# Kernel tuning notes

Measured on AMD Instinct MI355X. Metric: run time of the kernel, lower is better.

The kernel has to match this reference:

```python
import jax, jax.numpy as jnp
import numpy as np

MARGIN = 0.5
EPS = 1e-6  # torch F.pairwise_distance eps, added to the difference


def _make_indices(B, seed=0):
    rng = np.random.default_rng(seed)
    i1 = np.empty(B, dtype=np.int64)
    i2 = np.empty(B, dtype=np.int64)
    for i in range(B):
        a, b = rng.choice(B, size=2, replace=False)
        while a == i or b == i:
            a, b = rng.choice(B, size=2, replace=False)
        i1[i], i2[i] = a, b
    return i1, i2


def setup_inputs() -> dict:
    key = jax.random.key(0)
    k1, k2 = jax.random.split(key)
    B, D = 8192, 4096
    features = jax.random.normal(k1, (B, D), dtype=jnp.float32)
    label = jax.random.uniform(k2, (B, 1), dtype=jnp.float32) * 200.0  # bone-age-like months
    i1, i2 = _make_indices(B)
    return {
        "features": features,
        "label": label,
        "idx1": jnp.asarray(i1),
        "idx2": jnp.asarray(i2),
    }


def reference(features, label, idx1, idx2):
    # features: [B, D], label: [B, 1]
    a = features
    t1 = features[idx1]                                   # [B, D]
    t2 = features[idx2]                                   # [B, D]
    # L1Loss(reduction='sum') on per-sample labels
    d1 = jnp.sum(jnp.abs(label - label[idx1]), axis=-1)   # [B]
    d2 = jnp.sum(jnp.abs(label - label[idx2]), axis=-1)   # [B]
    # if d1 >= d2: near = t2, far = t1 else near = t1, far = t2
    swap = (d1 >= d2)[:, None]
    near = jnp.where(swap, t2, t1)
    far = jnp.where(swap, t1, t2)
    # TripletMarginLoss(margin=0.5, p=2); per-sample inputs are 1-D vectors,
    # so each call's 'mean' reduction is over a single element (identity).
    dn = jnp.sqrt(jnp.sum((a - near + EPS) ** 2, axis=-1))  # [B]
    df = jnp.sqrt(jnp.sum((a - far + EPS) ** 2, axis=-1))   # [B]
    per_sample = jnp.maximum(dn - df + MARGIN, 0.0)
    # loss is always >= 0, so the `if loss >= 0` accumulates every sample.
    return jnp.sum(per_sample)
```

## Files before the change

kernel.cpp:

```cpp
#include <hip/hip_runtime.h>

#define FEAT_D 4096
#define MARGIN_F 0.5f
#define EPS_F 1e-6f

__global__ __launch_bounds__(256) void triplet_loss_kernel(
    const float* __restrict__ features,
    const float* __restrict__ label,
    const int* __restrict__ idx1,
    const int* __restrict__ idx2,
    float* __restrict__ partials)
{
    const int row = blockIdx.x;
    const int tid = threadIdx.x;
    const int i1 = idx1[row];
    const int i2 = idx2[row];

    const float4* a  = reinterpret_cast<const float4*>(features + (size_t)row * FEAT_D) + tid;
    const float4* t1 = reinterpret_cast<const float4*>(features + (size_t)i1  * FEAT_D) + tid;
    const float4* t2 = reinterpret_cast<const float4*>(features + (size_t)i2  * FEAT_D) + tid;

    float s1 = 0.f, s2 = 0.f;
#pragma unroll
    for (int k = 0; k < 4; ++k) {
        const float4 va = a[k * 256];
        const float4 v1 = t1[k * 256];
        const float4 v2 = t2[k * 256];
        float d;
        d = va.x - v1.x + EPS_F; s1 += d * d;
        d = va.y - v1.y + EPS_F; s1 += d * d;
        d = va.z - v1.z + EPS_F; s1 += d * d;
        d = va.w - v1.w + EPS_F; s1 += d * d;
        d = va.x - v2.x + EPS_F; s2 += d * d;
        d = va.y - v2.y + EPS_F; s2 += d * d;
        d = va.z - v2.z + EPS_F; s2 += d * d;
        d = va.w - v2.w + EPS_F; s2 += d * d;
    }

#pragma unroll
    for (int off = 32; off > 0; off >>= 1) {
        s1 += __shfl_down(s1, off, 64);
        s2 += __shfl_down(s2, off, 64);
    }

    __shared__ float sh1[4], sh2[4];
    const int wave = tid >> 6;
    const int lane = tid & 63;
    if (lane == 0) { sh1[wave] = s1; sh2[wave] = s2; }
    __syncthreads();

    if (tid == 0) {
        const float S1 = sh1[0] + sh1[1] + sh1[2] + sh1[3];
        const float S2 = sh2[0] + sh2[1] + sh2[2] + sh2[3];
        const float lab = label[row];
        const float d1 = fabsf(lab - label[i1]);
        const float d2 = fabsf(lab - label[i2]);
        const bool swap = (d1 >= d2);
        const float sn = swap ? S2 : S1;
        const float sf = swap ? S1 : S2;
        const float loss = fmaxf(sqrtf(sn) - sqrtf(sf) + MARGIN_F, 0.f);
        partials[row] = loss;
    }
}

__global__ __launch_bounds__(256) void reduce_kernel(
    const float* __restrict__ partials, float* __restrict__ out, int n)
{
    const int tid = threadIdx.x;
    float s = 0.f;
    const float4* p4 = reinterpret_cast<const float4*>(partials);
    for (int i = tid; i < n / 4; i += 256) {
        const float4 v = p4[i];
        s += (v.x + v.y) + (v.z + v.w);
    }
#pragma unroll
    for (int off = 32; off > 0; off >>= 1)
        s += __shfl_down(s, off, 64);

    __shared__ float sh[4];
    const int wave = tid >> 6;
    const int lane = tid & 63;
    if (lane == 0) sh[wave] = s;
    __syncthreads();
    if (tid == 0) out[0] = sh[0] + sh[1] + sh[2] + sh[3];
}

extern "C" void kernel_launch(void* const* d_in, const int* in_sizes, int n_in,
                              void* d_out, int out_size, void* d_ws, size_t ws_size,
                              hipStream_t stream) {
    const float* features = (const float*)d_in[0];
    const float* label    = (const float*)d_in[1];
    const int*   idx1     = (const int*)d_in[2];
    const int*   idx2     = (const int*)d_in[3];
    float* out      = (float*)d_out;
    float* partials = (float*)d_ws;

    const int B = in_sizes[1];

    triplet_loss_kernel<<<B, 256, 0, stream>>>(features, label, idx1, idx2, partials);
    reduce_kernel<<<1, 256, 0, stream>>>(partials, out, B);
}
```

Before: 67.40 us.

## Process four rows per block with double-buffered register prefetch

Each block now handles four anchor rows and loads the next row's anchor and two target rows into a second register buffer while the current row is reduced. Sched barriers keep the load issue ahead of the compute. The goal is more memory-level parallelism per wave and less per-block launch and sync overhead. The cost is higher register pressure from 24 float4 buffers, and a quarter as many blocks. The final reduction kernel is also widened to 1024 threads.

```diff
diff --git a/kernel.cpp b/kernel.cpp
--- a/kernel.cpp
+++ b/kernel.cpp
@@ -3,6 +3,8 @@
 #define FEAT_D 4096
 #define MARGIN_F 0.5f
 #define EPS_F 1e-6f
+#define ROWS_PER_BLK 4
+
 
 __global__ __launch_bounds__(256) void triplet_loss_kernel(
     const float* __restrict__ features,
@@ -11,65 +13,86 @@
     const int* __restrict__ idx2,
     float* __restrict__ partials)
 {
-    const int row = blockIdx.x;
     const int tid = threadIdx.x;
-    const int i1 = idx1[row];
-    const int i2 = idx2[row];
+    const int row0 = blockIdx.x * ROWS_PER_BLK;
 
-    const float4* a  = reinterpret_cast<const float4*>(features + (size_t)row * FEAT_D) + tid;
-    const float4* t1 = reinterpret_cast<const float4*>(features + (size_t)i1  * FEAT_D) + tid;
-    const float4* t2 = reinterpret_cast<const float4*>(features + (size_t)i2  * FEAT_D) + tid;
+    __shared__ float sh1[ROWS_PER_BLK][4], sh2[ROWS_PER_BLK][4];
 
-    float s1 = 0.f, s2 = 0.f;
-#pragma unroll
-    for (int k = 0; k < 4; ++k) {
-        const float4 va = a[k * 256];
-        const float4 v1 = t1[k * 256];
-        const float4 v2 = t2[k * 256];
-        float d;
-        d = va.x - v1.x + EPS_F; s1 += d * d;
-        d = va.y - v1.y + EPS_F; s1 += d * d;
-        d = va.z - v1.z + EPS_F; s1 += d * d;
-        d = va.w - v1.w + EPS_F; s1 += d * d;
-        d = va.x - v2.x + EPS_F; s2 += d * d;
-        d = va.y - v2.y + EPS_F; s2 += d * d;
-        d = va.z - v2.z + EPS_F; s2 += d * d;
-        d = va.w - v2.w + EPS_F; s2 += d * d;
+    float4 bufA[12], bufB[12];
+
+#define ISSUE(BUF, R)                                                          \
+    {                                                                          \
+        const int rr_ = (R);                                                   \
+        const int j1_ = idx1[rr_], j2_ = idx2[rr_];                            \
+        const float4* pa_ = reinterpret_cast<const float4*>(features + (size_t)rr_ * FEAT_D) + tid; \
+        const float4* p1_ = reinterpret_cast<const float4*>(features + (size_t)j1_ * FEAT_D) + tid; \
+        const float4* p2_ = reinterpret_cast<const float4*>(features + (size_t)j2_ * FEAT_D) + tid; \
+        _Pragma("unroll")                                                      \
+        for (int k = 0; k < 4; ++k) BUF[k]     = pa_[k * 256];                 \
+        _Pragma("unroll")                                                      \
+        for (int k = 0; k < 4; ++k) BUF[4 + k] = p1_[k * 256];                 \
+        _Pragma("unroll")                                                      \
+        for (int k = 0; k < 4; ++k) BUF[8 + k] = p2_[k * 256];                 \
+    }                                                                          \
+    __builtin_amdgcn_sched_barrier(0);
+
+#define COMPUTE(BUF, SLOT)                                                     \
+    {                                                                          \
+        float s1_ = 0.f, s2_ = 0.f;                                            \
+        _Pragma("unroll")                                                      \
+        for (int k = 0; k < 4; ++k) {                                          \
+            float d_;                                                          \
+            d_ = BUF[k].x - BUF[4+k].x + EPS_F; s1_ += d_ * d_;                \
+            d_ = BUF[k].y - BUF[4+k].y + EPS_F; s1_ += d_ * d_;                \
+            d_ = BUF[k].z - BUF[4+k].z + EPS_F; s1_ += d_ * d_;                \
+            d_ = BUF[k].w - BUF[4+k].w + EPS_F; s1_ += d_ * d_;                \
+            d_ = BUF[k].x - BUF[8+k].x + EPS_F; s2_ += d_ * d_;                \
+            d_ = BUF[k].y - BUF[8+k].y + EPS_F; s2_ += d_ * d_;                \
+            d_ = BUF[k].z - BUF[8+k].z + EPS_F; s2_ += d_ * d_;                \
+            d_ = BUF[k].w - BUF[8+k].w + EPS_F; s2_ += d_ * d_;                \
+        }                                                                      \
+        _Pragma("unroll")                                                      \
+        for (int off = 32; off > 0; off >>= 1) {                               \
+            s1_ += __shfl_down(s1_, off, 64);                                  \
+            s2_ += __shfl_down(s2_, off, 64);                                  \
+        }                                                                      \
+        if ((tid & 63) == 0) { sh1[SLOT][tid >> 6] = s1_; sh2[SLOT][tid >> 6] = s2_; } \
     }
 
-#pragma unroll
-    for (int off = 32; off > 0; off >>= 1) {
-        s1 += __shfl_down(s1, off, 64);
-        s2 += __shfl_down(s2, off, 64);
-    }
+    ISSUE(bufA, row0)
+    ISSUE(bufB, row0 + 1)
+    COMPUTE(bufA, 0)
+    ISSUE(bufA, row0 + 2)
+    COMPUTE(bufB, 1)
+    ISSUE(bufB, row0 + 3)
+    COMPUTE(bufA, 2)
+    COMPUTE(bufB, 3)
 
-    __shared__ float sh1[4], sh2[4];
-    const int wave = tid >> 6;
-    const int lane = tid & 63;
-    if (lane == 0) { sh1[wave] = s1; sh2[wave] = s2; }
     __syncthreads();
 
-    if (tid == 0) {
-        const float S1 = sh1[0] + sh1[1] + sh1[2] + sh1[3];
-        const float S2 = sh2[0] + sh2[1] + sh2[2] + sh2[3];
-        const float lab = label[row];
-        const float d1 = fabsf(lab - label[i1]);
-        const float d2 = fabsf(lab - label[i2]);
+    if (tid < ROWS_PER_BLK) {
+        const int r = row0 + tid;
+        const float S1 = sh1[tid][0] + sh1[tid][1] + sh1[tid][2] + sh1[tid][3];
+        const float S2 = sh2[tid][0] + sh2[tid][1] + sh2[tid][2] + sh2[tid][3];
+        const float lab = label[r];
+        const float d1 = fabsf(lab - label[idx1[r]]);
+        const float d2 = fabsf(lab - label[idx2[r]]);
         const bool swap = (d1 >= d2);
         const float sn = swap ? S2 : S1;
         const float sf = swap ? S1 : S2;
-        const float loss = fmaxf(sqrtf(sn) - sqrtf(sf) + MARGIN_F, 0.f);
-        partials[row] = loss;
+        partials[r] = fmaxf(sqrtf(sn) - sqrtf(sf) + MARGIN_F, 0.f);
     }
+#undef ISSUE
+#undef COMPUTE
 }
 
-__global__ __launch_bounds__(256) void reduce_kernel(
+__global__ __launch_bounds__(1024) void reduce_kernel(
     const float* __restrict__ partials, float* __restrict__ out, int n)
 {
     const int tid = threadIdx.x;
     float s = 0.f;
     const float4* p4 = reinterpret_cast<const float4*>(partials);
-    for (int i = tid; i < n / 4; i += 256) {
+    for (int i = tid; i < n / 4; i += 1024) {
         const float4 v = p4[i];
         s += (v.x + v.y) + (v.z + v.w);
     }
@@ -77,12 +100,17 @@
     for (int off = 32; off > 0; off >>= 1)
         s += __shfl_down(s, off, 64);
 
-    __shared__ float sh[4];
+    __shared__ float sh[16];
     const int wave = tid >> 6;
     const int lane = tid & 63;
     if (lane == 0) sh[wave] = s;
     __syncthreads();
-    if (tid == 0) out[0] = sh[0] + sh[1] + sh[2] + sh[3];
+    if (tid == 0) {
+        float t = 0.f;
+#pragma unroll
+        for (int w = 0; w < 16; ++w) t += sh[w];
+        out[0] = t;
+    }
 }
 
 extern "C" void kernel_launch(void* const* d_in, const int* in_sizes, int n_in,
@@ -97,6 +125,6 @@
 
     const int B = in_sizes[1];
 
-    triplet_loss_kernel<<<B, 256, 0, stream>>>(features, label, idx1, idx2, partials);
-    reduce_kernel<<<1, 256, 0, stream>>>(partials, out, B);
+    triplet_loss_kernel<<<B / ROWS_PER_BLK, 256, 0, stream>>>(features, label, idx1, idx2, partials);
+    reduce_kernel<<<1, 1024, 0, stream>>>(partials, out, B);
 }
```

Result: faster. 63.38 us (-6.0%).
